# Performance work log

Hardware: AMD Instinct MI355X
Metric: run time of the kernel (lower is better)

Reference implementation:

```python
import jax, jax.numpy as jnp
import numpy as np

HID = 256  # hardcoded LSTM hidden size in the module


def _lstm_cell(x, h, c, W_ih, W_hh, b_ih, b_hh):
    # PyTorch gate order: i, f, g, o. x,h: [1,HID]; W_*: [4H,HID]; b_*: [4H]
    gates = x @ W_ih.T + h @ W_hh.T + b_ih + b_hh  # [1,4H]
    i, f, g, o = jnp.split(gates, 4, axis=-1)
    c_new = jax.nn.sigmoid(f) * c + jax.nn.sigmoid(i) * jnp.tanh(g)
    h_new = jax.nn.sigmoid(o) * jnp.tanh(c_new)
    return h_new, c_new


def setup_inputs() -> dict:
    key = jax.random.key(0)
    ks = jax.random.split(key, 9)
    s = 0.05
    return {
        "zm_1": jax.random.normal(ks[0], (1, HID), jnp.float32) * s,
        "W_ih": jax.random.normal(ks[1], (4 * HID, HID), jnp.float32) * s,
        "W_hh": jax.random.normal(ks[2], (4 * HID, HID), jnp.float32) * s,
        "b_ih": jax.random.normal(ks[3], (4 * HID,), jnp.float32) * s,
        "b_hh": jax.random.normal(ks[4], (4 * HID,), jnp.float32) * s,
        "W_loc": jax.random.normal(ks[5], (64, HID), jnp.float32) * s,
        "b_loc": jax.random.normal(ks[6], (64,), jnp.float32) * s,
        "W_scale": jax.random.normal(ks[7], (64, HID), jnp.float32) * s,
        "b_scale": jax.random.normal(ks[8], (64,), jnp.float32) * s,
        "K": 7,
        "batch_size": 32768,
    }


def reference(zm_1, W_ih, W_hh, b_ih, b_hh, W_loc, b_loc, W_scale, b_scale, K, batch_size):
    zm_size = W_loc.shape[0]
    h0 = jnp.zeros((1, HID), zm_1.dtype)
    c0 = jnp.zeros((1, HID), zm_1.dtype)

    def step(carry, _):
        x, h, c = carry
        h_new, c_new = _lstm_cell(x, h, c, W_ih, W_hh, b_ih, b_hh)
        # LSTM output z == h_new; it is also the next step's input
        return (h_new, h_new, c_new), h_new

    _, zs = jax.lax.scan(step, (zm_1, h0, c0), None, length=K - 1)  # [K-1,1,HID]
    p_z = jnp.concatenate([zm_1[None], zs], axis=0).reshape(K, HID)  # [K,HID]

    loc = p_z @ W_loc.T + b_loc        # [K,zm]
    scale = p_z @ W_scale.T + b_scale  # [K,zm]
    # repeat over batch dim -> [K*batch_size, zm]
    loc = jnp.broadcast_to(loc[:, None, :], (K, batch_size, zm_size)).reshape(-1, zm_size)
    scale = jnp.broadcast_to(scale[:, None, :], (K, batch_size, zm_size)).reshape(-1, zm_size)
    return loc, scale
```

## Files before the change

### kernel.cpp

```cpp
#include <hip/hip_runtime.h>
#include <cstdint>
#include <cstddef>

#define HID    256
#define G4     1024
#define KSTEPS 7
#define NBLK   4
#define TPB    1024
#define ZM     64
#define BATCH  32768

typedef float f32x4 __attribute__((ext_vector_type(4)));

#define WS_GATES_F 256
#define WS_TAB_F   (256 + 6 * G4)

__device__ __forceinline__ void grid_barrier(unsigned* cnt) {
    __syncthreads();
    if (threadIdx.x == 0) {
        __hip_atomic_fetch_add(cnt, 1u, __ATOMIC_ACQ_REL, __HIP_MEMORY_SCOPE_AGENT);
        while (__hip_atomic_load(cnt, __ATOMIC_ACQUIRE, __HIP_MEMORY_SCOPE_AGENT) < (unsigned)NBLK) {
            __builtin_amdgcn_s_sleep(1);
        }
    }
    __syncthreads();
}

__device__ __forceinline__ float sigf(float x)  { return 1.0f / (1.0f + __expf(-x)); }
__device__ __forceinline__ float tanhf_fast(float x) { return 1.0f - 2.0f / (__expf(2.0f * x) + 1.0f); }

__device__ __forceinline__ float dot4(f32x4 a, f32x4 b) {
    return a.x * b.x + a.y * b.y + a.z * b.z + a.w * b.w;
}

__global__ __launch_bounds__(TPB) void lstm_kernel(
    const float* __restrict__ zm1,
    const float* __restrict__ Wih, const float* __restrict__ Whh,
    const float* __restrict__ bih, const float* __restrict__ bhh,
    const float* __restrict__ Wloc, const float* __restrict__ bloc,
    const float* __restrict__ Wsc,  const float* __restrict__ bsc,
    float* __restrict__ ws)
{
    __shared__ float pz[KSTEPS][HID];
    __shared__ float act[G4];
    const int t    = threadIdx.x;
    const int b    = blockIdx.x;
    const int rloc = t >> 2;
    const int q    = t & 3;
    const int row  = b * (TPB / 4) + rloc;

    unsigned* cnts = (unsigned*)ws;
    float* gates = ws + WS_GATES_F;
    float* tab   = ws + WS_TAB_F;

    if (t < HID) pz[0][t] = zm1[t];
    __syncthreads();

    const float bias = bih[row] + bhh[row];

    f32x4 wsum[16];
    {
        const f32x4* a4 = (const f32x4*)(Wih + (size_t)row * HID);
        const f32x4* x4 = (const f32x4*)(&pz[0][0]);
        float part = 0.f;
        #pragma unroll
        for (int kk = 0; kk < 16; ++kk) {
            const int idx = q + 4 * kk;
            f32x4 a = a4[idx];
            wsum[kk] = a;
            part += dot4(a, x4[idx]);
        }
        const f32x4* c4 = (const f32x4*)(Whh + (size_t)row * HID);
        #pragma unroll
        for (int kk = 0; kk < 16; ++kk) {
            wsum[kk] += c4[q + 4 * kk];
        }
        part += __shfl_xor(part, 1);
        part += __shfl_xor(part, 2);
        if (q == 0)
            __hip_atomic_store(&gates[row], part + bias,
                               __ATOMIC_RELAXED, __HIP_MEMORY_SCOPE_AGENT);
    }

    float creg = 0.f;
    #pragma unroll 1
    for (int s = 1; s <= KSTEPS - 1; ++s) {
        grid_barrier(&cnts[(s - 1) * 32]);
        {
            const float* gs = gates + (size_t)(s - 1) * G4;
            float g = __hip_atomic_load(&gs[t], __ATOMIC_RELAXED, __HIP_MEMORY_SCOPE_AGENT);
            act[t] = (t >= 512 && t < 768) ? tanhf_fast(g) : sigf(g);
        }
        __syncthreads();
        if (t < HID) {
            creg = act[HID + t] * creg + act[t] * act[2 * HID + t];
            pz[s][t] = act[3 * HID + t] * tanhf_fast(creg);
        }
        __syncthreads();
        if (s == KSTEPS - 1) break;
        const f32x4* h4 = (const f32x4*)(&pz[s][0]);
        float part = 0.f;
        #pragma unroll
        for (int kk = 0; kk < 16; ++kk) {
            part += dot4(wsum[kk], h4[q + 4 * kk]);
        }
        part += __shfl_xor(part, 1);
        part += __shfl_xor(part, 2);
        if (q == 0)
            __hip_atomic_store(&gates[(size_t)s * G4 + row], part + bias,
                               __ATOMIC_RELAXED, __HIP_MEMORY_SCOPE_AGENT);
    }

    const int g    = b * TPB + t;
    const int slot = g >> 2;
    if (slot < 2 * KSTEPS * ZM) {
        const int which = slot / (KSTEPS * ZM);
        const int r     = slot - which * (KSTEPS * ZM);
        const int m     = r >> 6;
        const int j     = r & 63;
        const float* W  = which ? Wsc : Wloc;
        const float  bb = which ? bsc[j] : bloc[j];
        const f32x4* w4 = (const f32x4*)(W + (size_t)j * HID);
        const f32x4* p4 = (const f32x4*)(&pz[m][0]);
        float acc = 0.f;
        #pragma unroll
        for (int kk = 0; kk < 16; ++kk) {
            const int idx = q + 4 * kk;
            acc += dot4(w4[idx], p4[idx]);
        }
        acc += __shfl_xor(acc, 1);
        acc += __shfl_xor(acc, 2);
        if (q == 0) tab[slot] = acc + bb;
    }
}

__global__ __launch_bounds__(256) void bcast_kernel(
    const float* __restrict__ tab, f32x4* __restrict__ out)
{
    const int bid   = blockIdx.x;
    const int wm    = bid >> 7;
    const int chunk = bid & 127;
    const f32x4* t4 = (const f32x4*)tab;
    const f32x4 v = t4[wm * 16 + (threadIdx.x & 15)];
    size_t base = (size_t)wm * (BATCH * ZM / 4) + (size_t)chunk * 4096 + threadIdx.x;
    #pragma unroll
    for (int k = 0; k < 16; ++k) {
        __builtin_nontemporal_store(v, &out[base + (size_t)k * 256]);
    }
}

extern "C" void kernel_launch(void* const* d_in, const int* in_sizes, int n_in,
                              void* d_out, int out_size, void* d_ws, size_t ws_size,
                              hipStream_t stream) {
    const float* zm1  = (const float*)d_in[0];
    const float* Wih  = (const float*)d_in[1];
    const float* Whh  = (const float*)d_in[2];
    const float* bih  = (const float*)d_in[3];
    const float* bhh  = (const float*)d_in[4];
    const float* Wloc = (const float*)d_in[5];
    const float* bloc = (const float*)d_in[6];
    const float* Wsc  = (const float*)d_in[7];
    const float* bsc  = (const float*)d_in[8];
    float* ws = (float*)d_ws;

    (void)hipMemsetAsync(d_ws, 0, 1024, stream);

    lstm_kernel<<<NBLK, TPB, 0, stream>>>(zm1, Wih, Whh, bih, bhh,
                                          Wloc, bloc, Wsc, bsc, ws);

    bcast_kernel<<<14 * 128, 256, 0, stream>>>(ws + WS_TAB_F, (f32x4*)d_out);
}
```

Measured before the change: 179.0 us.

## Replace persistent grid-barrier LSTM kernel with per-step kernel launches

The single persistent 4-block kernel used atomic grid barriers between recurrence steps. It is replaced by an init kernel that precomputes the summed weights and first gates across 256 blocks, five per-step kernels over 64 blocks, and a final projection kernel. Kernel boundaries now order the steps, which removes the spin-wait barriers and the memset and spreads each step over more CUs. The cost is several extra launches and reloading the summed weights from global memory at every step.

New measurement: 165.0 us. 1.09x faster.

```diff
diff --git a/kernel.cpp b/kernel.cpp
--- a/kernel.cpp
+++ b/kernel.cpp
@@ -3,135 +3,121 @@
 #include <cstddef>
 
 #define HID    256
-#define G4     1024
+#define NROW   1024
 #define KSTEPS 7
-#define NBLK   4
-#define TPB    1024
 #define ZM     64
 #define BATCH  32768
 
 typedef float f32x4 __attribute__((ext_vector_type(4)));
 
-#define WS_GATES_F 256
-#define WS_TAB_F   (256 + 6 * G4)
+#define WS_GATES 0
+#define WS_C     (6 * NROW)
+#define WS_PZ    (6 * NROW + 7 * HID)
+#define WS_TAB   (6 * NROW + 14 * HID)
+#define WS_WSUM  (6 * NROW + 14 * HID + 896)
 
-__device__ __forceinline__ void grid_barrier(unsigned* cnt) {
-    __syncthreads();
-    if (threadIdx.x == 0) {
-        __hip_atomic_fetch_add(cnt, 1u, __ATOMIC_ACQ_REL, __HIP_MEMORY_SCOPE_AGENT);
-        while (__hip_atomic_load(cnt, __ATOMIC_ACQUIRE, __HIP_MEMORY_SCOPE_AGENT) < (unsigned)NBLK) {
-            __builtin_amdgcn_s_sleep(1);
-        }
-    }
-    __syncthreads();
-}
-
-__device__ __forceinline__ float sigf(float x)  { return 1.0f / (1.0f + __expf(-x)); }
+__device__ __forceinline__ float sigf(float x)       { return 1.0f / (1.0f + __expf(-x)); }
 __device__ __forceinline__ float tanhf_fast(float x) { return 1.0f - 2.0f / (__expf(2.0f * x) + 1.0f); }
 
 __device__ __forceinline__ float dot4(f32x4 a, f32x4 b) {
     return a.x * b.x + a.y * b.y + a.z * b.z + a.w * b.w;
 }
 
-__global__ __launch_bounds__(TPB) void lstm_kernel(
+__global__ __launch_bounds__(256) void init_kernel(
     const float* __restrict__ zm1,
     const float* __restrict__ Wih, const float* __restrict__ Whh,
     const float* __restrict__ bih, const float* __restrict__ bhh,
+    float* __restrict__ ws)
+{
+    const int t = threadIdx.x, b = blockIdx.x;
+    f32x4*       wsum4 = (f32x4*)(ws + WS_WSUM);
+    const f32x4* a4    = (const f32x4*)Wih;
+    const f32x4* c4    = (const f32x4*)Whh;
+    const int id = b * 256 + t;
+    wsum4[id] = a4[id] + c4[id];
+
+    if (b == 0) {
+        ws[WS_PZ + t] = zm1[t];
+        ws[WS_C + t]  = 0.0f;
+    }
+    if (b < 64) {
+        const int row = b * 16 + (t >> 4);
+        const int l16 = t & 15;
+        const f32x4* w4 = (const f32x4*)(Wih + (size_t)row * HID);
+        const f32x4* x4 = (const f32x4*)zm1;
+        float part = 0.f;
+        #pragma unroll
+        for (int kk = 0; kk < 4; ++kk) part += dot4(w4[l16 * 4 + kk], x4[l16 * 4 + kk]);
+        part += __shfl_xor(part, 1);
+        part += __shfl_xor(part, 2);
+        part += __shfl_xor(part, 4);
+        part += __shfl_xor(part, 8);
+        if (l16 == 0) ws[WS_GATES + row] = part + bih[row] + bhh[row];
+    }
+}
+
+__global__ __launch_bounds__(256) void step_kernel(
+    const float* __restrict__ bih, const float* __restrict__ bhh,
+    float* __restrict__ ws, int s)
+{
+    __shared__ float hsh[HID];
+    const int t = threadIdx.x, b = blockIdx.x;
+    {
+        const float* gp = ws + WS_GATES + (size_t)(s - 1) * NROW;
+        float gi = gp[t], gf = gp[HID + t], gg = gp[2 * HID + t], go = gp[3 * HID + t];
+        float cp = ws[WS_C + (size_t)(s - 1) * HID + t];
+        float cn = sigf(gf) * cp + sigf(gi) * tanhf_fast(gg);
+        float h  = sigf(go) * tanhf_fast(cn);
+        ws[WS_C + (size_t)s * HID + t] = cn;
+        if (b == 0) ws[WS_PZ + (size_t)s * HID + t] = h;
+        hsh[t] = h;
+    }
+    __syncthreads();
+    const int row = b * 16 + (t >> 4);
+    const int l16 = t & 15;
+    const f32x4* w4 = (const f32x4*)(ws + WS_WSUM + (size_t)row * HID);
+    const f32x4* h4 = (const f32x4*)hsh;
+    float part = 0.f;
+    #pragma unroll
+    for (int kk = 0; kk < 4; ++kk) part += dot4(w4[l16 * 4 + kk], h4[l16 * 4 + kk]);
+    part += __shfl_xor(part, 1);
+    part += __shfl_xor(part, 2);
+    part += __shfl_xor(part, 4);
+    part += __shfl_xor(part, 8);
+    if (l16 == 0) ws[WS_GATES + (size_t)s * NROW + row] = part + bih[row] + bhh[row];
+}
+
+__global__ __launch_bounds__(256) void final_kernel(
     const float* __restrict__ Wloc, const float* __restrict__ bloc,
     const float* __restrict__ Wsc,  const float* __restrict__ bsc,
     float* __restrict__ ws)
 {
-    __shared__ float pz[KSTEPS][HID];
-    __shared__ float act[G4];
-    const int t    = threadIdx.x;
-    const int b    = blockIdx.x;
-    const int rloc = t >> 2;
-    const int q    = t & 3;
-    const int row  = b * (TPB / 4) + rloc;
-
-    unsigned* cnts = (unsigned*)ws;
-    float* gates = ws + WS_GATES_F;
-    float* tab   = ws + WS_TAB_F;
-
-    if (t < HID) pz[0][t] = zm1[t];
+    __shared__ float hsh[HID];
+    const int t = threadIdx.x, b = blockIdx.x;
+    {
+        const float* gp = ws + WS_GATES + (size_t)5 * NROW;
+        float gi = gp[t], gf = gp[HID + t], gg = gp[2 * HID + t], go = gp[3 * HID + t];
+        float cp = ws[WS_C + (size_t)5 * HID + t];
+        float cn = sigf(gf) * cp + sigf(gi) * tanhf_fast(gg);
+        hsh[t] = sigf(go) * tanhf_fast(cn);
+    }
     __syncthreads();
-
-    const float bias = bih[row] + bhh[row];
-
-    f32x4 wsum[16];
-    {
-        const f32x4* a4 = (const f32x4*)(Wih + (size_t)row * HID);
-        const f32x4* x4 = (const f32x4*)(&pz[0][0]);
-        float part = 0.f;
-        #pragma unroll
-        for (int kk = 0; kk < 16; ++kk) {
-            const int idx = q + 4 * kk;
-            f32x4 a = a4[idx];
-            wsum[kk] = a;
-            part += dot4(a, x4[idx]);
-        }
-        const f32x4* c4 = (const f32x4*)(Whh + (size_t)row * HID);
-        #pragma unroll
-        for (int kk = 0; kk < 16; ++kk) {
-            wsum[kk] += c4[q + 4 * kk];
-        }
-        part += __shfl_xor(part, 1);
-        part += __shfl_xor(part, 2);
-        if (q == 0)
-            __hip_atomic_store(&gates[row], part + bias,
-                               __ATOMIC_RELAXED, __HIP_MEMORY_SCOPE_AGENT);
-    }
-
-    float creg = 0.f;
-    #pragma unroll 1
-    for (int s = 1; s <= KSTEPS - 1; ++s) {
-        grid_barrier(&cnts[(s - 1) * 32]);
-        {
-            const float* gs = gates + (size_t)(s - 1) * G4;
-            float g = __hip_atomic_load(&gs[t], __ATOMIC_RELAXED, __HIP_MEMORY_SCOPE_AGENT);
-            act[t] = (t >= 512 && t < 768) ? tanhf_fast(g) : sigf(g);
-        }
-        __syncthreads();
-        if (t < HID) {
-            creg = act[HID + t] * creg + act[t] * act[2 * HID + t];
-            pz[s][t] = act[3 * HID + t] * tanhf_fast(creg);
-        }
-        __syncthreads();
-        if (s == KSTEPS - 1) break;
-        const f32x4* h4 = (const f32x4*)(&pz[s][0]);
-        float part = 0.f;
-        #pragma unroll
-        for (int kk = 0; kk < 16; ++kk) {
-            part += dot4(wsum[kk], h4[q + 4 * kk]);
-        }
-        part += __shfl_xor(part, 1);
-        part += __shfl_xor(part, 2);
-        if (q == 0)
-            __hip_atomic_store(&gates[(size_t)s * G4 + row], part + bias,
-                               __ATOMIC_RELAXED, __HIP_MEMORY_SCOPE_AGENT);
-    }
-
-    const int g    = b * TPB + t;
-    const int slot = g >> 2;
-    if (slot < 2 * KSTEPS * ZM) {
-        const int which = slot / (KSTEPS * ZM);
-        const int r     = slot - which * (KSTEPS * ZM);
-        const int m     = r >> 6;
-        const int j     = r & 63;
-        const float* W  = which ? Wsc : Wloc;
-        const float  bb = which ? bsc[j] : bloc[j];
-        const f32x4* w4 = (const f32x4*)(W + (size_t)j * HID);
-        const f32x4* p4 = (const f32x4*)(&pz[m][0]);
-        float acc = 0.f;
-        #pragma unroll
-        for (int kk = 0; kk < 16; ++kk) {
-            const int idx = q + 4 * kk;
-            acc += dot4(w4[idx], p4[idx]);
-        }
-        acc += __shfl_xor(acc, 1);
-        acc += __shfl_xor(acc, 2);
-        if (q == 0) tab[slot] = acc + bb;
-    }
+    const int wm    = b;
+    const int which = wm / KSTEPS;
+    const int m     = wm % KSTEPS;
+    const int j     = t >> 2;
+    const int q     = t & 3;
+    const float* W  = which ? Wsc : Wloc;
+    const float  bb = which ? bsc[j] : bloc[j];
+    const f32x4* w4 = (const f32x4*)(W + (size_t)j * HID);
+    const f32x4* p4 = (m == 6) ? (const f32x4*)hsh
+                               : (const f32x4*)(ws + WS_PZ + (size_t)m * HID);
+    float acc = 0.f;
+    #pragma unroll
+    for (int kk = 0; kk < 16; ++kk) acc += dot4(w4[q * 16 + kk], p4[q * 16 + kk]);
+    acc += __shfl_xor(acc, 1);
+    acc += __shfl_xor(acc, 2);
+    if (q == 0) ws[WS_TAB + wm * ZM + j] = acc + bb;
 }
 
 __global__ __launch_bounds__(256) void bcast_kernel(
@@ -163,10 +149,9 @@
     const float* bsc  = (const float*)d_in[8];
     float* ws = (float*)d_ws;
 
-    (void)hipMemsetAsync(d_ws, 0, 1024, stream);
-
-    lstm_kernel<<<NBLK, TPB, 0, stream>>>(zm1, Wih, Whh, bih, bhh,
-                                          Wloc, bloc, Wsc, bsc, ws);
-
-    bcast_kernel<<<14 * 128, 256, 0, stream>>>(ws + WS_TAB_F, (f32x4*)d_out);
+    init_kernel<<<256, 256, 0, stream>>>(zm1, Wih, Whh, bih, bhh, ws);
+    for (int s = 1; s <= 5; ++s)
+        step_kernel<<<64, 256, 0, stream>>>(bih, bhh, ws, s);
+    final_kernel<<<14, 256, 0, stream>>>(Wloc, bloc, Wsc, bsc, ws);
+    bcast_kernel<<<14 * 128, 256, 0, stream>>>(ws + WS_TAB, (f32x4*)d_out);
 }
```
